# Optimization experiments

Measured on AMD Instinct MI355X. Metric: run time of the kernel, lower is better.

Reference implementation:

```python
import jax, jax.numpy as jnp
import numpy as np

EDGE_DIM = 64
NODE_DIM = 64
IN_DIM = NODE_DIM * 2 + EDGE_DIM  # 192
N_NODES = 50000
N_EDGES = 800000


def setup_inputs() -> dict:
    key = jax.random.key(0)
    k = jax.random.split(key, 8)
    node_feats = jax.random.normal(k[0], (N_NODES, NODE_DIM), dtype=jnp.float32)
    edge_feats = jax.random.normal(k[1], (N_EDGES, EDGE_DIM), dtype=jnp.float32)
    edge_index = jax.random.randint(k[2], (2, N_EDGES), 0, N_NODES, dtype=jnp.int64)
    s1 = 1.0 / np.sqrt(IN_DIM)
    W1 = jax.random.uniform(k[3], (IN_DIM, IN_DIM), jnp.float32, -s1, s1)
    b1 = jax.random.uniform(k[4], (IN_DIM,), jnp.float32, -s1, s1)
    gamma = jnp.ones((IN_DIM,), jnp.float32)
    beta = jnp.zeros((IN_DIM,), jnp.float32)
    W2 = jax.random.uniform(k[5], (IN_DIM, EDGE_DIM), jnp.float32, -s1, s1)
    b2 = jax.random.uniform(k[6], (EDGE_DIM,), jnp.float32, -s1, s1)
    return {"node_feats": node_feats, "edge_feats": edge_feats, "edge_index": edge_index,
            "W1": W1, "b1": b1, "gamma": gamma, "beta": beta, "W2": W2, "b2": b2}


def _layernorm(x, gamma, beta, eps=1e-5):
    mu = jnp.mean(x, axis=-1, keepdims=True)
    var = jnp.mean(jnp.square(x - mu), axis=-1, keepdims=True)
    return (x - mu) * jax.lax.rsqrt(var + eps) * gamma + beta


def reference(node_feats, edge_feats, edge_index, W1, b1, gamma, beta, W2, b2):
    row, col = edge_index[0], edge_index[1]
    # [E, 2*node_dim + edge_dim]
    x = jnp.concatenate([node_feats[row], node_feats[col], edge_feats], axis=-1)
    h = jnp.matmul(x, W1) + b1
    h = jax.nn.relu(_layernorm(h, gamma, beta))
    return jnp.matmul(h, W2) + b2 + edge_feats
```

## Files before the change

### kernel.cpp

```cpp
#include <hip/hip_runtime.h>
#include <hip/hip_bf16.h>

#define N_EDGES   800000
#define IN_DIM    192
#define BM        128
#define NT1       12
#define NT2       4
#define KS        6
#define XPITCH    200

typedef __attribute__((ext_vector_type(8))) short short8;
typedef __attribute__((ext_vector_type(4))) float f32x4;

__device__ __forceinline__ ushort f2b(float f) {
    unsigned int u = __float_as_uint(f);
    unsigned int r = (u + 0x7FFFu + ((u >> 16) & 1u)) >> 16;
    return (ushort)r;
}

__global__ __launch_bounds__(512, 2)
void fused_edge_kernel(const float* __restrict__ nf, const float* __restrict__ ef,
                       const int* __restrict__ ei,
                       const float* __restrict__ W1, const float* __restrict__ b1,
                       const float* __restrict__ gamma, const float* __restrict__ beta,
                       const float* __restrict__ W2, const float* __restrict__ b2,
                       float* __restrict__ out)
{
    __shared__ __align__(16) ushort Wl[49152];
    __shared__ __align__(16) ushort XH[BM * XPITCH];
    __shared__ int idxs[BM * 2];

    const int tid  = threadIdx.x;
    const int w    = tid >> 6;
    const int lane = tid & 63;
    const int lrow = lane & 15;
    const int lg   = lane >> 4;

    for (int i = tid; i < 6144; i += 512) {
        int l = i & 63, ts = i >> 6;
        const float* Wsrc; int t, s, N;
        if (ts < 72) { t = ts / 6; s = ts - t * 6; Wsrc = W1; N = 192; }
        else { int u2 = ts - 72; t = u2 / 6; s = u2 - t * 6; Wsrc = W2; N = 64; }
        int kb  = s * 32 + (l >> 4) * 8;
        int col = t * 16 + (l & 15);
        const float* p = Wsrc + (size_t)kb * N + col;
        ushort tmp[8];
        #pragma unroll
        for (int j = 0; j < 8; ++j) tmp[j] = f2b(p[j * N]);
        uint4 d;
        d.x = tmp[0] | ((unsigned)tmp[1] << 16);
        d.y = tmp[2] | ((unsigned)tmp[3] << 16);
        d.z = tmp[4] | ((unsigned)tmp[5] << 16);
        d.w = tmp[6] | ((unsigned)tmp[7] << 16);
        *(uint4*)&Wl[(size_t)i * 8] = d;
    }

    float b1v[NT1], gv[NT1], bev[NT1], b2v[NT2];
    #pragma unroll
    for (int t = 0; t < NT1; ++t) {
        int c = t * 16 + lrow;
        b1v[t] = b1[c]; gv[t] = gamma[c]; bev[t] = beta[c];
    }
    #pragma unroll
    for (int t = 0; t < NT2; ++t) b2v[t] = b2[t * 16 + lrow];

    const int ntile = N_EDGES / BM;
    for (int tile = blockIdx.x; tile < ntile; tile += gridDim.x) {
        const int e0 = tile * BM;

        __syncthreads();
        if (tid < 256) {
            int which = tid >> 7, le = tid & 127;
            idxs[le * 2 + which] = ei[which * N_EDGES + e0 + le];
        }
        __syncthreads();

        #pragma unroll
        for (int j = 0; j < 12; ++j) {
            int fi = j * 512 + tid;
            int le = fi / 48;
            int c4 = fi - le * 48;
            const float* src;
            if (c4 < 16)      src = nf + (size_t)idxs[le * 2]     * 64 + c4 * 4;
            else if (c4 < 32) src = nf + (size_t)idxs[le * 2 + 1] * 64 + (c4 - 16) * 4;
            else              src = ef + (size_t)(e0 + le)        * 64 + (c4 - 32) * 4;
            float4 v = *(const float4*)src;
            uint2 pk;
            pk.x = f2b(v.x) | ((unsigned)f2b(v.y) << 16);
            pk.y = f2b(v.z) | ((unsigned)f2b(v.w) << 16);
            *(uint2*)&XH[le * XPITCH + c4 * 4] = pk;
        }
        __syncthreads();

        f32x4 acc[NT1];
        #pragma unroll
        for (int t = 0; t < NT1; ++t) { acc[t][0]=0.f; acc[t][1]=0.f; acc[t][2]=0.f; acc[t][3]=0.f; }
        {
            const ushort* arow = &XH[(w * 16 + lrow) * XPITCH];
            #pragma unroll
            for (int k = 0; k < KS; ++k) {
                short8 a = *(const short8*)(arow + k * 32 + lg * 8);
                #pragma unroll
                for (int t = 0; t < NT1; ++t) {
                    short8 b = *(const short8*)&Wl[((t * KS + k) * 64 + lane) * 8];
                    acc[t] = __builtin_amdgcn_mfma_f32_16x16x32_bf16(a, b, acc[t], 0, 0, 0);
                }
            }
        }

        float mu[4], rs[4];
        #pragma unroll
        for (int r = 0; r < 4; ++r) {
            float s = 0.f, q = 0.f;
            #pragma unroll
            for (int t = 0; t < NT1; ++t) {
                float v = acc[t][r] + b1v[t];
                acc[t][r] = v;
                s += v; q += v * v;
            }
            #pragma unroll
            for (int m = 1; m < 16; m <<= 1) {
                s += __shfl_xor(s, m, 64);
                q += __shfl_xor(q, m, 64);
            }
            float mean = s * (1.f / 192.f);
            float var  = q * (1.f / 192.f) - mean * mean;
            mu[r] = mean;
            rs[r] = rsqrtf(var + 1e-5f);
        }
        #pragma unroll
        for (int t = 0; t < NT1; ++t) {
            #pragma unroll
            for (int r = 0; r < 4; ++r) {
                float v = (acc[t][r] - mu[r]) * rs[r] * gv[t] + bev[t];
                v = fmaxf(v, 0.f);
                XH[(w * 16 + lg * 4 + r) * XPITCH + t * 16 + lrow] = f2b(v);
            }
        }

        f32x4 acc2[NT2];
        #pragma unroll
        for (int t = 0; t < NT2; ++t) { acc2[t][0]=0.f; acc2[t][1]=0.f; acc2[t][2]=0.f; acc2[t][3]=0.f; }
        {
            const ushort* hrow = &XH[(w * 16 + lrow) * XPITCH];
            #pragma unroll
            for (int k = 0; k < KS; ++k) {
                short8 a = *(const short8*)(hrow + k * 32 + lg * 8);
                #pragma unroll
                for (int t = 0; t < NT2; ++t) {
                    short8 b = *(const short8*)&Wl[(4608 + (t * KS + k) * 64 + lane) * 8];
                    acc2[t] = __builtin_amdgcn_mfma_f32_16x16x32_bf16(a, b, acc2[t], 0, 0, 0);
                }
            }
        }

        #pragma unroll
        for (int t = 0; t < NT2; ++t) {
            #pragma unroll
            for (int r = 0; r < 4; ++r) {
                int le2 = w * 16 + lg * 4 + r;
                size_t off = (size_t)(e0 + le2) * 64 + t * 16 + lrow;
                out[off] = acc2[t][r] + b2v[t] + ef[off];
            }
        }
    }
}

extern "C" void kernel_launch(void* const* d_in, const int* in_sizes, int n_in,
                              void* d_out, int out_size, void* d_ws, size_t ws_size,
                              hipStream_t stream) {
    const float* nf    = (const float*)d_in[0];
    const float* ef    = (const float*)d_in[1];
    const int*   ei    = (const int*)d_in[2];
    const float* W1    = (const float*)d_in[3];
    const float* b1    = (const float*)d_in[4];
    const float* gamma = (const float*)d_in[5];
    const float* beta  = (const float*)d_in[6];
    const float* W2    = (const float*)d_in[7];
    const float* b2    = (const float*)d_in[8];
    float* out = (float*)d_out;

    hipLaunchKernelGGL(fused_edge_kernel, dim3(256), dim3(512), 0, stream,
                       nf, ef, ei, W1, b1, gamma, beta, W2, b2, out);
}
```

Baseline: 553.8 us.

## Hold weights in registers, split tiles across warps by column, prefetch next tile

The bf16 weight fragments move from shared memory into per-warp registers. Each warp now owns 64 rows and a 48-column slice of the first matmul, and a 16-column slice of the second. Because each warp sees only part of a row, the LayerNorm statistics are reduced across warps through shared memory, which adds two block barriers. The gather of the next tile's node and edge features is issued into registers before the second matmul so it overlaps compute, at the cost of much higher register pressure under launch bounds of 512 threads and 2 blocks.

```diff
diff --git a/kernel.cpp b/kernel.cpp
--- a/kernel.cpp
+++ b/kernel.cpp
@@ -1,21 +1,18 @@
 #include <hip/hip_runtime.h>
 #include <hip/hip_bf16.h>
 
-#define N_EDGES   800000
-#define IN_DIM    192
-#define BM        128
-#define NT1       12
-#define NT2       4
-#define KS        6
-#define XPITCH    200
+#define NE      800000
+#define BM      128
+#define XPITCH  200
+#define NTILE   (NE / BM)
+#define GRID    256
 
 typedef __attribute__((ext_vector_type(8))) short short8;
 typedef __attribute__((ext_vector_type(4))) float f32x4;
 
 __device__ __forceinline__ ushort f2b(float f) {
     unsigned int u = __float_as_uint(f);
-    unsigned int r = (u + 0x7FFFu + ((u >> 16) & 1u)) >> 16;
-    return (ushort)r;
+    return (ushort)((u + 0x7FFFu + ((u >> 16) & 1u)) >> 16);
 }
 
 __global__ __launch_bounds__(512, 2)
@@ -26,64 +23,61 @@
                        const float* __restrict__ W2, const float* __restrict__ b2,
                        float* __restrict__ out)
 {
-    __shared__ __align__(16) ushort Wl[49152];
     __shared__ __align__(16) ushort XH[BM * XPITCH];
-    __shared__ int idxs[BM * 2];
+    __shared__ float2 sums[BM * 4];
+    __shared__ float2 musr[BM];
+    __shared__ int    idxs[BM * 2];
 
     const int tid  = threadIdx.x;
     const int w    = tid >> 6;
     const int lane = tid & 63;
     const int lrow = lane & 15;
     const int lg   = lane >> 4;
-
-    for (int i = tid; i < 6144; i += 512) {
-        int l = i & 63, ts = i >> 6;
-        const float* Wsrc; int t, s, N;
-        if (ts < 72) { t = ts / 6; s = ts - t * 6; Wsrc = W1; N = 192; }
-        else { int u2 = ts - 72; t = u2 / 6; s = u2 - t * 6; Wsrc = W2; N = 64; }
-        int kb  = s * 32 + (l >> 4) * 8;
-        int col = t * 16 + (l & 15);
-        const float* p = Wsrc + (size_t)kb * N + col;
-        ushort tmp[8];
-        #pragma unroll
-        for (int j = 0; j < 8; ++j) tmp[j] = f2b(p[j * N]);
-        uint4 d;
-        d.x = tmp[0] | ((unsigned)tmp[1] << 16);
-        d.y = tmp[2] | ((unsigned)tmp[3] << 16);
-        d.z = tmp[4] | ((unsigned)tmp[5] << 16);
-        d.w = tmp[6] | ((unsigned)tmp[7] << 16);
-        *(uint4*)&Wl[(size_t)i * 8] = d;
-    }
-
-    float b1v[NT1], gv[NT1], bev[NT1], b2v[NT2];
+    const int wr   = w >> 2;
+    const int wc   = w & 3;
+    const int rowbase = wr * 64;
+
+    short8 w1f[3][6], w2f[6];
     #pragma unroll
-    for (int t = 0; t < NT1; ++t) {
-        int c = t * 16 + lrow;
-        b1v[t] = b1[c]; gv[t] = gamma[c]; bev[t] = beta[c];
-    }
+    for (int tl = 0; tl < 3; ++tl) {
+        int c = wc * 48 + tl * 16 + lrow;
+        #pragma unroll
+        for (int k = 0; k < 6; ++k) {
+            const float* p = W1 + (size_t)(k * 32 + lg * 8) * 192 + c;
+            #pragma unroll
+            for (int j = 0; j < 8; ++j) w1f[tl][k][j] = (short)f2b(p[(size_t)j * 192]);
+        }
+    }
+    {
+        int c2 = wc * 16 + lrow;
+        #pragma unroll
+        for (int k = 0; k < 6; ++k) {
+            const float* p = W2 + (size_t)(k * 32 + lg * 8) * 64 + c2;
+            #pragma unroll
+            for (int j = 0; j < 8; ++j) w2f[k][j] = (short)f2b(p[(size_t)j * 64]);
+        }
+    }
+    float b1v[3], gv[3], bev[3];
     #pragma unroll
-    for (int t = 0; t < NT2; ++t) b2v[t] = b2[t * 16 + lrow];
-
-    const int ntile = N_EDGES / BM;
-    for (int tile = blockIdx.x; tile < ntile; tile += gridDim.x) {
+    for (int tl = 0; tl < 3; ++tl) {
+        int c = wc * 48 + tl * 16 + lrow;
+        b1v[tl] = b1[c]; gv[tl] = gamma[c]; bev[tl] = beta[c];
+    }
+    const float b2v = b2[wc * 16 + lrow];
+
+    int tile = blockIdx.x;
+    {
         const int e0 = tile * BM;
-
-        __syncthreads();
-        if (tid < 256) {
-            int which = tid >> 7, le = tid & 127;
-            idxs[le * 2 + which] = ei[which * N_EDGES + e0 + le];
-        }
-        __syncthreads();
-
+        if (tid < 256) idxs[(tid & 127) * 2 + (tid >> 7)] = ei[(tid >> 7) * NE + e0 + (tid & 127)];
+        __syncthreads();
         #pragma unroll
         for (int j = 0; j < 12; ++j) {
-            int fi = j * 512 + tid;
-            int le = fi / 48;
-            int c4 = fi - le * 48;
+            int fi = j * 512 + tid, le = fi / 48, c4 = fi - le * 48;
+            int2 rc = *(const int2*)&idxs[le * 2];
             const float* src;
-            if (c4 < 16)      src = nf + (size_t)idxs[le * 2]     * 64 + c4 * 4;
-            else if (c4 < 32) src = nf + (size_t)idxs[le * 2 + 1] * 64 + (c4 - 16) * 4;
-            else              src = ef + (size_t)(e0 + le)        * 64 + (c4 - 32) * 4;
+            if (c4 < 16)      src = nf + (size_t)rc.x * 64 + c4 * 4;
+            else if (c4 < 32) src = nf + (size_t)rc.y * 64 + (c4 - 16) * 4;
+            else              src = ef + (size_t)(e0 + le) * 64 + (c4 - 32) * 4;
             float4 v = *(const float4*)src;
             uint2 pk;
             pk.x = f2b(v.x) | ((unsigned)f2b(v.y) << 16);
@@ -91,78 +85,140 @@
             *(uint2*)&XH[le * XPITCH + c4 * 4] = pk;
         }
         __syncthreads();
-
-        f32x4 acc[NT1];
-        #pragma unroll
-        for (int t = 0; t < NT1; ++t) { acc[t][0]=0.f; acc[t][1]=0.f; acc[t][2]=0.f; acc[t][3]=0.f; }
-        {
-            const ushort* arow = &XH[(w * 16 + lrow) * XPITCH];
-            #pragma unroll
-            for (int k = 0; k < KS; ++k) {
-                short8 a = *(const short8*)(arow + k * 32 + lg * 8);
-                #pragma unroll
-                for (int t = 0; t < NT1; ++t) {
-                    short8 b = *(const short8*)&Wl[((t * KS + k) * 64 + lane) * 8];
-                    acc[t] = __builtin_amdgcn_mfma_f32_16x16x32_bf16(a, b, acc[t], 0, 0, 0);
+    }
+
+    for (; tile < NTILE; tile += GRID) {
+        const int e0 = tile * BM;
+        const int tnext = tile + GRID;
+        const bool hasNext = tnext < NTILE;
+        const int e1 = hasNext ? tnext * BM : 0;
+
+        int idxnew = 0;
+        if (hasNext && tid < 256) idxnew = ei[(tid >> 7) * NE + e1 + (tid & 127)];
+
+        f32x4 acc1[4][3];
+        #pragma unroll
+        for (int m = 0; m < 4; ++m)
+            #pragma unroll
+            for (int tl = 0; tl < 3; ++tl)
+                acc1[m][tl] = (f32x4){0.f, 0.f, 0.f, 0.f};
+        #pragma unroll
+        for (int k = 0; k < 6; ++k) {
+            short8 a[4];
+            #pragma unroll
+            for (int m = 0; m < 4; ++m)
+                a[m] = *(const short8*)&XH[(rowbase + m * 16 + lrow) * XPITCH + k * 32 + lg * 8];
+            #pragma unroll
+            for (int m = 0; m < 4; ++m)
+                #pragma unroll
+                for (int tl = 0; tl < 3; ++tl)
+                    acc1[m][tl] = __builtin_amdgcn_mfma_f32_16x16x32_bf16(a[m], w1f[tl][k], acc1[m][tl], 0, 0, 0);
+        }
+
+        #pragma unroll
+        for (int m = 0; m < 4; ++m) {
+            #pragma unroll
+            for (int rr = 0; rr < 4; ++rr) {
+                float s = 0.f, q = 0.f;
+                #pragma unroll
+                for (int tl = 0; tl < 3; ++tl) {
+                    float v = acc1[m][tl][rr] + b1v[tl];
+                    acc1[m][tl][rr] = v;
+                    s += v; q += v * v;
                 }
-            }
-        }
-
-        float mu[4], rs[4];
-        #pragma unroll
-        for (int r = 0; r < 4; ++r) {
-            float s = 0.f, q = 0.f;
-            #pragma unroll
-            for (int t = 0; t < NT1; ++t) {
-                float v = acc[t][r] + b1v[t];
-                acc[t][r] = v;
-                s += v; q += v * v;
-            }
-            #pragma unroll
-            for (int m = 1; m < 16; m <<= 1) {
-                s += __shfl_xor(s, m, 64);
-                q += __shfl_xor(q, m, 64);
-            }
+                #pragma unroll
+                for (int msk = 1; msk < 16; msk <<= 1) {
+                    s += __shfl_xor(s, msk, 64);
+                    q += __shfl_xor(q, msk, 64);
+                }
+                if (lrow == 0)
+                    sums[(rowbase + m * 16 + lg * 4 + rr) * 4 + wc] = make_float2(s, q);
+            }
+        }
+        __syncthreads();
+        if (tid < 128) {
+            float2 a0 = sums[tid * 4 + 0], a1 = sums[tid * 4 + 1];
+            float2 a2 = sums[tid * 4 + 2], a3 = sums[tid * 4 + 3];
+            float s = a0.x + a1.x + a2.x + a3.x;
+            float q = a0.y + a1.y + a2.y + a3.y;
             float mean = s * (1.f / 192.f);
             float var  = q * (1.f / 192.f) - mean * mean;
-            mu[r] = mean;
-            rs[r] = rsqrtf(var + 1e-5f);
-        }
-        #pragma unroll
-        for (int t = 0; t < NT1; ++t) {
-            #pragma unroll
-            for (int r = 0; r < 4; ++r) {
-                float v = (acc[t][r] - mu[r]) * rs[r] * gv[t] + bev[t];
-                v = fmaxf(v, 0.f);
-                XH[(w * 16 + lg * 4 + r) * XPITCH + t * 16 + lrow] = f2b(v);
-            }
-        }
-
-        f32x4 acc2[NT2];
-        #pragma unroll
-        for (int t = 0; t < NT2; ++t) { acc2[t][0]=0.f; acc2[t][1]=0.f; acc2[t][2]=0.f; acc2[t][3]=0.f; }
-        {
-            const ushort* hrow = &XH[(w * 16 + lrow) * XPITCH];
-            #pragma unroll
-            for (int k = 0; k < KS; ++k) {
-                short8 a = *(const short8*)(hrow + k * 32 + lg * 8);
-                #pragma unroll
-                for (int t = 0; t < NT2; ++t) {
-                    short8 b = *(const short8*)&Wl[(4608 + (t * KS + k) * 64 + lane) * 8];
-                    acc2[t] = __builtin_amdgcn_mfma_f32_16x16x32_bf16(a, b, acc2[t], 0, 0, 0);
+            musr[tid] = make_float2(mean, rsqrtf(var + 1e-5f));
+        }
+        __syncthreads();
+
+        #pragma unroll
+        for (int m = 0; m < 4; ++m) {
+            #pragma unroll
+            for (int rr = 0; rr < 4; ++rr) {
+                int row = rowbase + m * 16 + lg * 4 + rr;
+                float2 mr = musr[row];
+                #pragma unroll
+                for (int tl = 0; tl < 3; ++tl) {
+                    float v = (acc1[m][tl][rr] - mr.x) * mr.y * gv[tl] + bev[tl];
+                    XH[row * XPITCH + wc * 48 + tl * 16 + lrow] = f2b(fmaxf(v, 0.f));
                 }
             }
         }
-
-        #pragma unroll
-        for (int t = 0; t < NT2; ++t) {
-            #pragma unroll
-            for (int r = 0; r < 4; ++r) {
-                int le2 = w * 16 + lg * 4 + r;
-                size_t off = (size_t)(e0 + le2) * 64 + t * 16 + lrow;
-                out[off] = acc2[t][r] + b2v[t] + ef[off];
-            }
-        }
+        if (hasNext && tid < 256) idxs[(tid & 127) * 2 + (tid >> 7)] = idxnew;
+        __syncthreads();
+
+        float4 xv[12];
+        if (hasNext) {
+            #pragma unroll
+            for (int j = 0; j < 12; ++j) {
+                int fi = j * 512 + tid, le = fi / 48, c4 = fi - le * 48;
+                int2 rc = *(const int2*)&idxs[le * 2];
+                const float* src;
+                if (c4 < 16)      src = nf + (size_t)rc.x * 64 + c4 * 4;
+                else if (c4 < 32) src = nf + (size_t)rc.y * 64 + (c4 - 16) * 4;
+                else              src = ef + (size_t)(e1 + le) * 64 + (c4 - 32) * 4;
+                xv[j] = *(const float4*)src;
+            }
+        }
+        float efv[16];
+        #pragma unroll
+        for (int m = 0; m < 4; ++m)
+            #pragma unroll
+            for (int rr = 0; rr < 4; ++rr) {
+                int row = rowbase + m * 16 + lg * 4 + rr;
+                efv[m * 4 + rr] = ef[(size_t)(e0 + row) * 64 + wc * 16 + lrow];
+            }
+
+        f32x4 acc2[4];
+        #pragma unroll
+        for (int m = 0; m < 4; ++m) acc2[m] = (f32x4){0.f, 0.f, 0.f, 0.f};
+        #pragma unroll
+        for (int k = 0; k < 6; ++k) {
+            short8 h[4];
+            #pragma unroll
+            for (int m = 0; m < 4; ++m)
+                h[m] = *(const short8*)&XH[(rowbase + m * 16 + lrow) * XPITCH + k * 32 + lg * 8];
+            #pragma unroll
+            for (int m = 0; m < 4; ++m)
+                acc2[m] = __builtin_amdgcn_mfma_f32_16x16x32_bf16(h[m], w2f[k], acc2[m], 0, 0, 0);
+        }
+
+        #pragma unroll
+        for (int m = 0; m < 4; ++m)
+            #pragma unroll
+            for (int rr = 0; rr < 4; ++rr) {
+                int row = rowbase + m * 16 + lg * 4 + rr;
+                out[(size_t)(e0 + row) * 64 + wc * 16 + lrow] = acc2[m][rr] + b2v + efv[m * 4 + rr];
+            }
+
+        __syncthreads();
+        if (hasNext) {
+            #pragma unroll
+            for (int j = 0; j < 12; ++j) {
+                int fi = j * 512 + tid, le = fi / 48, c4 = fi - le * 48;
+                uint2 pk;
+                pk.x = f2b(xv[j].x) | ((unsigned)f2b(xv[j].y) << 16);
+                pk.y = f2b(xv[j].z) | ((unsigned)f2b(xv[j].w) << 16);
+                *(uint2*)&XH[le * XPITCH + c4 * 4] = pk;
+            }
+        }
+        __syncthreads();
     }
 }
 
@@ -180,6 +236,6 @@
     const float* b2    = (const float*)d_in[8];
     float* out = (float*)d_out;
 
-    hipLaunchKernelGGL(fused_edge_kernel, dim3(256), dim3(512), 0, stream,
+    hipLaunchKernelGGL(fused_edge_kernel, dim3(GRID), dim3(512), 0, stream,
                        nf, ef, ei, W1, b1, gamma, beta, W2, b2, out);
 }
```

Result: slower. 724.8 us (+30.9%).

## Pre-pack weights to global memory and run barrier-free per-wave 32-edge tiles

Applied to the files above, without the earlier changes.

Weight bf16 packing moves out of the main kernel into a separate pack kernel that writes MFMA-ready fragments to the workspace. The main kernel then reads B fragments straight from global memory (L2-cached) instead of LDS. Each wave independently processes 32-edge tiles with a private LDS slice, which removes all block-level __syncthreads. The grid grows to 2048 blocks of 256 threads so more waves are resident to hide gather latency. The trade is repeated global/L2 weight fragment loads per tile in place of LDS reads.

```diff
diff --git a/kernel.cpp b/kernel.cpp
--- a/kernel.cpp
+++ b/kernel.cpp
@@ -1,168 +1,157 @@
 #include <hip/hip_runtime.h>
-#include <hip/hip_bf16.h>
 
-#define N_EDGES   800000
-#define IN_DIM    192
-#define BM        128
-#define NT1       12
-#define NT2       4
-#define KS        6
-#define XPITCH    200
+#define NE     800000
+#define NWT    25000
+#define GRID   2048
+#define HP     200
 
 typedef __attribute__((ext_vector_type(8))) short short8;
 typedef __attribute__((ext_vector_type(4))) float f32x4;
 
 __device__ __forceinline__ ushort f2b(float f) {
-    unsigned int u = __float_as_uint(f);
-    unsigned int r = (u + 0x7FFFu + ((u >> 16) & 1u)) >> 16;
-    return (ushort)r;
+    unsigned u = __float_as_uint(f);
+    return (ushort)((u + 0x7FFFu + ((u >> 16) & 1u)) >> 16);
 }
 
-__global__ __launch_bounds__(512, 2)
-void fused_edge_kernel(const float* __restrict__ nf, const float* __restrict__ ef,
-                       const int* __restrict__ ei,
-                       const float* __restrict__ W1, const float* __restrict__ b1,
-                       const float* __restrict__ gamma, const float* __restrict__ beta,
-                       const float* __restrict__ W2, const float* __restrict__ b2,
-                       float* __restrict__ out)
+__global__ void pack_w(const float* __restrict__ W1, const float* __restrict__ W2,
+                       uint4* __restrict__ wsW)
 {
-    __shared__ __align__(16) ushort Wl[49152];
-    __shared__ __align__(16) ushort XH[BM * XPITCH];
-    __shared__ int idxs[BM * 2];
+    int i = blockIdx.x * 256 + threadIdx.x;
+    int lane = i & 63, e = i >> 6;
+    const float* W; int N, t, k;
+    if (e < 72) { W = W1; N = 192; t = e / 6; k = e - t * 6; }
+    else        { int e2 = e - 72; W = W2; N = 64; t = e2 / 6; k = e2 - t * 6; }
+    const float* p = W + (size_t)(k * 32 + (lane >> 4) * 8) * N + t * 16 + (lane & 15);
+    ushort u[8];
+    #pragma unroll
+    for (int j = 0; j < 8; ++j) u[j] = f2b(p[(size_t)j * N]);
+    uint4 d;
+    d.x = u[0] | ((unsigned)u[1] << 16);
+    d.y = u[2] | ((unsigned)u[3] << 16);
+    d.z = u[4] | ((unsigned)u[5] << 16);
+    d.w = u[6] | ((unsigned)u[7] << 16);
+    wsW[i] = d;
+}
 
-    const int tid  = threadIdx.x;
-    const int w    = tid >> 6;
-    const int lane = tid & 63;
-    const int lrow = lane & 15;
-    const int lg   = lane >> 4;
+__global__ __launch_bounds__(256, 3)
+void edge_kernel(const float* __restrict__ nf, const float* __restrict__ ef,
+                 const int* __restrict__ ei,
+                 const float* __restrict__ b1g, const float* __restrict__ gammag,
+                 const float* __restrict__ betag, const float* __restrict__ b2g,
+                 const uint4* __restrict__ wsW, float* __restrict__ out)
+{
+    __shared__ ushort Xs[4][32 * HP];
+    const int tid = threadIdx.x, w = tid >> 6, lane = tid & 63;
+    const int lrow = lane & 15, lg = lane >> 4, le = lane & 31;
+    ushort* X = Xs[w];
 
-    for (int i = tid; i < 6144; i += 512) {
-        int l = i & 63, ts = i >> 6;
-        const float* Wsrc; int t, s, N;
-        if (ts < 72) { t = ts / 6; s = ts - t * 6; Wsrc = W1; N = 192; }
-        else { int u2 = ts - 72; t = u2 / 6; s = u2 - t * 6; Wsrc = W2; N = 64; }
-        int kb  = s * 32 + (l >> 4) * 8;
-        int col = t * 16 + (l & 15);
-        const float* p = Wsrc + (size_t)kb * N + col;
-        ushort tmp[8];
-        #pragma unroll
-        for (int j = 0; j < 8; ++j) tmp[j] = f2b(p[j * N]);
-        uint4 d;
-        d.x = tmp[0] | ((unsigned)tmp[1] << 16);
-        d.y = tmp[2] | ((unsigned)tmp[3] << 16);
-        d.z = tmp[4] | ((unsigned)tmp[5] << 16);
-        d.w = tmp[6] | ((unsigned)tmp[7] << 16);
-        *(uint4*)&Wl[(size_t)i * 8] = d;
-    }
-
-    float b1v[NT1], gv[NT1], bev[NT1], b2v[NT2];
+    float b1v[12], gv[12], bev[12], b2v[4];
     #pragma unroll
-    for (int t = 0; t < NT1; ++t) {
-        int c = t * 16 + lrow;
-        b1v[t] = b1[c]; gv[t] = gamma[c]; bev[t] = beta[c];
+    for (int t = 0; t < 12; ++t) {
+        b1v[t] = b1g[t * 16 + lrow];
+        gv[t]  = gammag[t * 16 + lrow];
+        bev[t] = betag[t * 16 + lrow];
     }
     #pragma unroll
-    for (int t = 0; t < NT2; ++t) b2v[t] = b2[t * 16 + lrow];
+    for (int t = 0; t < 4; ++t) b2v[t] = b2g[t * 16 + lrow];
 
-    const int ntile = N_EDGES / BM;
-    for (int tile = blockIdx.x; tile < ntile; tile += gridDim.x) {
-        const int e0 = tile * BM;
+    for (int wt = blockIdx.x * 4 + w; wt < NWT; wt += GRID * 4) {
+        const int e0 = wt * 32;
+        int idxreg = ei[(lane >> 5) * NE + e0 + le];
+        int ir = __shfl(idxreg, le, 64);
+        int ic = __shfl(idxreg, le + 32, 64);
 
-        __syncthreads();
-        if (tid < 256) {
-            int which = tid >> 7, le = tid & 127;
-            idxs[le * 2 + which] = ei[which * N_EDGES + e0 + le];
-        }
-        __syncthreads();
-
+        const float* pr = nf + (size_t)ir * 64;
+        const float* pc = nf + (size_t)ic * 64;
+        const float* pe = ef + (size_t)(e0 + le) * 64;
         #pragma unroll
-        for (int j = 0; j < 12; ++j) {
-            int fi = j * 512 + tid;
-            int le = fi / 48;
-            int c4 = fi - le * 48;
+        for (int j = 0; j < 24; ++j) {
+            int c4 = 2 * j + (lane >> 5);
             const float* src;
-            if (c4 < 16)      src = nf + (size_t)idxs[le * 2]     * 64 + c4 * 4;
-            else if (c4 < 32) src = nf + (size_t)idxs[le * 2 + 1] * 64 + (c4 - 16) * 4;
-            else              src = ef + (size_t)(e0 + le)        * 64 + (c4 - 32) * 4;
+            if (j < 8)       src = pr + c4 * 4;
+            else if (j < 16) src = pc + (c4 - 16) * 4;
+            else             src = pe + (c4 - 32) * 4;
             float4 v = *(const float4*)src;
             uint2 pk;
             pk.x = f2b(v.x) | ((unsigned)f2b(v.y) << 16);
             pk.y = f2b(v.z) | ((unsigned)f2b(v.w) << 16);
-            *(uint2*)&XH[le * XPITCH + c4 * 4] = pk;
+            *(uint2*)&X[le * HP + c4 * 4] = pk;
         }
-        __syncthreads();
 
-        f32x4 acc[NT1];
+        f32x4 acc1[2][12];
         #pragma unroll
-        for (int t = 0; t < NT1; ++t) { acc[t][0]=0.f; acc[t][1]=0.f; acc[t][2]=0.f; acc[t][3]=0.f; }
-        {
-            const ushort* arow = &XH[(w * 16 + lrow) * XPITCH];
+        for (int m = 0; m < 2; ++m)
             #pragma unroll
-            for (int k = 0; k < KS; ++k) {
-                short8 a = *(const short8*)(arow + k * 32 + lg * 8);
+            for (int t = 0; t < 12; ++t)
+                acc1[m][t] = (f32x4){0.f, 0.f, 0.f, 0.f};
+        #pragma unroll
+        for (int ks = 0; ks < 6; ++ks) {
+            short8 a0 = *(const short8*)&X[(lrow)      * HP + ks * 32 + lg * 8];
+            short8 a1 = *(const short8*)&X[(16 + lrow) * HP + ks * 32 + lg * 8];
+            #pragma unroll
+            for (int t = 0; t < 12; ++t) {
+                short8 bf = *(const short8*)(wsW + (size_t)(t * 6 + ks) * 64 + lane);
+                acc1[0][t] = __builtin_amdgcn_mfma_f32_16x16x32_bf16(a0, bf, acc1[0][t], 0, 0, 0);
+                acc1[1][t] = __builtin_amdgcn_mfma_f32_16x16x32_bf16(a1, bf, acc1[1][t], 0, 0, 0);
+            }
+        }
+
+        #pragma unroll
+        for (int m = 0; m < 2; ++m) {
+            #pragma unroll
+            for (int rr = 0; rr < 4; ++rr) {
+                float s = 0.f, q = 0.f;
                 #pragma unroll
-                for (int t = 0; t < NT1; ++t) {
-                    short8 b = *(const short8*)&Wl[((t * KS + k) * 64 + lane) * 8];
-                    acc[t] = __builtin_amdgcn_mfma_f32_16x16x32_bf16(a, b, acc[t], 0, 0, 0);
+                for (int t = 0; t < 12; ++t) {
+                    float v = acc1[m][t][rr] + b1v[t];
+                    acc1[m][t][rr] = v;
+                    s += v; q += v * v;
+                }
+                #pragma unroll
+                for (int msk = 1; msk < 16; msk <<= 1) {
+                    s += __shfl_xor(s, msk, 64);
+                    q += __shfl_xor(q, msk, 64);
+                }
+                float mean = s * (1.f / 192.f);
+                float var  = q * (1.f / 192.f) - mean * mean;
+                float rsv  = rsqrtf(var + 1e-5f);
+                int row = m * 16 + lg * 4 + rr;
+                #pragma unroll
+                for (int t = 0; t < 12; ++t) {
+                    float v = (acc1[m][t][rr] - mean) * rsv * gv[t] + bev[t];
+                    X[row * HP + t * 16 + lrow] = f2b(fmaxf(v, 0.f));
                 }
             }
         }
 
-        float mu[4], rs[4];
+        f32x4 acc2[2][4];
         #pragma unroll
-        for (int r = 0; r < 4; ++r) {
-            float s = 0.f, q = 0.f;
+        for (int m = 0; m < 2; ++m)
             #pragma unroll
-            for (int t = 0; t < NT1; ++t) {
-                float v = acc[t][r] + b1v[t];
-                acc[t][r] = v;
-                s += v; q += v * v;
-            }
+            for (int t = 0; t < 4; ++t)
+                acc2[m][t] = (f32x4){0.f, 0.f, 0.f, 0.f};
+        #pragma unroll
+        for (int ks = 0; ks < 6; ++ks) {
+            short8 h0 = *(const short8*)&X[(lrow)      * HP + ks * 32 + lg * 8];
+            short8 h1 = *(const short8*)&X[(16 + lrow) * HP + ks * 32 + lg * 8];
             #pragma unroll
-            for (int m = 1; m < 16; m <<= 1) {
-                s += __shfl_xor(s, m, 64);
-                q += __shfl_xor(q, m, 64);
-            }
-            float mean = s * (1.f / 192.f);
-            float var  = q * (1.f / 192.f) - mean * mean;
-            mu[r] = mean;
-            rs[r] = rsqrtf(var + 1e-5f);
-        }
-        #pragma unroll
-        for (int t = 0; t < NT1; ++t) {
-            #pragma unroll
-            for (int r = 0; r < 4; ++r) {
-                float v = (acc[t][r] - mu[r]) * rs[r] * gv[t] + bev[t];
-                v = fmaxf(v, 0.f);
-                XH[(w * 16 + lg * 4 + r) * XPITCH + t * 16 + lrow] = f2b(v);
-            }
-        }
-
-        f32x4 acc2[NT2];
-        #pragma unroll
-        for (int t = 0; t < NT2; ++t) { acc2[t][0]=0.f; acc2[t][1]=0.f; acc2[t][2]=0.f; acc2[t][3]=0.f; }
-        {
-            const ushort* hrow = &XH[(w * 16 + lrow) * XPITCH];
-            #pragma unroll
-            for (int k = 0; k < KS; ++k) {
-                short8 a = *(const short8*)(hrow + k * 32 + lg * 8);
-                #pragma unroll
-                for (int t = 0; t < NT2; ++t) {
-                    short8 b = *(const short8*)&Wl[(4608 + (t * KS + k) * 64 + lane) * 8];
-                    acc2[t] = __builtin_amdgcn_mfma_f32_16x16x32_bf16(a, b, acc2[t], 0, 0, 0);
-                }
+            for (int t = 0; t < 4; ++t) {
+                short8 bf = *(const short8*)(wsW + (size_t)(72 + t * 6 + ks) * 64 + lane);
+                acc2[0][t] = __builtin_amdgcn_mfma_f32_16x16x32_bf16(h0, bf, acc2[0][t], 0, 0, 0);
+                acc2[1][t] = __builtin_amdgcn_mfma_f32_16x16x32_bf16(h1, bf, acc2[1][t], 0, 0, 0);
             }
         }
 
         #pragma unroll
-        for (int t = 0; t < NT2; ++t) {
+        for (int m = 0; m < 2; ++m)
             #pragma unroll
-            for (int r = 0; r < 4; ++r) {
-                int le2 = w * 16 + lg * 4 + r;
-                size_t off = (size_t)(e0 + le2) * 64 + t * 16 + lrow;
-                out[off] = acc2[t][r] + b2v[t] + ef[off];
-            }
-        }
+            for (int t = 0; t < 4; ++t)
+                #pragma unroll
+                for (int rr = 0; rr < 4; ++rr) {
+                    int row = m * 16 + lg * 4 + rr;
+                    size_t o = (size_t)(e0 + row) * 64 + t * 16 + lrow;
+                    out[o] = acc2[m][t][rr] + b2v[t] + ef[o];
+                }
     }
 }
 
@@ -179,7 +168,9 @@
     const float* W2    = (const float*)d_in[7];
     const float* b2    = (const float*)d_in[8];
     float* out = (float*)d_out;
+    uint4* wsW = (uint4*)d_ws;
 
-    hipLaunchKernelGGL(fused_edge_kernel, dim3(256), dim3(512), 0, stream,
-                       nf, ef, ei, W1, b1, gamma, beta, W2, b2, out);
+    hipLaunchKernelGGL(pack_w, dim3(24), dim3(256), 0, stream, W1, W2, wsW);
+    hipLaunchKernelGGL(edge_kernel, dim3(GRID), dim3(256), 0, stream,
+                       nf, ef, ei, b1, gamma, beta, b2, (const uint4*)wsW, out);
 }
```

Measured after the change: 1.493 ms. 2.7x slower.
